# Performance work log

Measured on AMD Instinct MI355X. Metric: run time of the kernel, lower is better.

Reference implementation:

```python
import jax, jax.numpy as jnp
import numpy as np

BORDER_POWER = 0.5
BORDER_WEIGHT = 1.0


def _distance_transform(targets):
    """Vertical two-pass (grassfire) min-plus distance transform along H.

    Matches torch: init penalty=H everywhere, 0 at target==1, then a downward
    pass d[i] = min(d[i], d[i-1]+1) followed by an upward pass
    d[i] = min(d[i], d[i+1]+1).
    """
    H = targets.shape[2]
    D = jnp.where(targets == 1, jnp.float32(0.0), jnp.float32(H))  # (N,C,H,W)
    Dh = jnp.moveaxis(D, 2, 0)  # (H, N, C, W)

    def step(carry, row):
        r = jnp.minimum(row, carry + 1.0)
        return r, r

    big = jnp.full_like(Dh[0], jnp.inf)  # inf+1=inf so first row is unchanged
    _, Dfwd = jax.lax.scan(step, big, Dh)
    _, Dbwd = jax.lax.scan(step, big, Dfwd, reverse=True)
    return jnp.moveaxis(Dbwd, 0, 2)  # back to (N,C,H,W)


def setup_inputs() -> dict:
    key = jax.random.key(0)
    k1, k2 = jax.random.split(key)
    predictions = jax.random.normal(k1, (32, 1, 1024, 1024), dtype=jnp.float32)
    targets = jax.random.randint(k2, (32, 1, 1024, 1024), 0, 2).astype(jnp.float32)
    return {"predictions": predictions, "targets": targets}


def reference(predictions, targets):
    # BCEWithLogitsLoss, mean reduction (numerically stable form)
    bce = jnp.mean(
        jnp.maximum(predictions, 0.0)
        - predictions * targets
        + jnp.log1p(jnp.exp(-jnp.abs(predictions)))
    )

    # Border criterion: hard-thresholded sigmoid predictions times distance map
    pred_bin = (jax.nn.sigmoid(predictions) > 0.5).astype(jnp.float32)
    dist = _distance_transform(targets)
    penalty = pred_bin * dist
    total = penalty.sum()
    count = jnp.sum(penalty != 0).astype(jnp.float32)
    border = jnp.where(total == 0, 0.0, total / jnp.maximum(count, 1.0))

    return bce + BORDER_WEIGHT * border ** BORDER_POWER
```

## Files before the change

### kernel.cpp

```cpp
#include <hip/hip_runtime.h>
#include <math.h>

#define HH   1024
#define WW   1024
#define NIMG 32
#define NBLK (NIMG * (WW / 32))
#define NT   512
#define BIGD (1<<20)
#define L2E  1.44269504088896340736f

#if __has_builtin(__builtin_amdgcn_exp2f)
#define EXP2F(x) __builtin_amdgcn_exp2f(x)
#else
#define EXP2F(x) exp2f(x)
#endif
#if __has_builtin(__builtin_amdgcn_logf)
#define LOG2F(x) __builtin_amdgcn_logf(x)
#else
#define LOG2F(x) log2f(x)
#endif


__global__ __launch_bounds__(NT, 8) void dtl_main(const float* __restrict__ pred,
                                                  const float* __restrict__ tgt,
                                                  double* __restrict__ bceP,
                                                  unsigned* __restrict__ totP,
                                                  unsigned* __restrict__ cntP) {
    __shared__ unsigned long long nibw[16][64];
    __shared__ int st_first[16][32];
    __shared__ int st_last[16][32];
    __shared__ float    red_f[NT];
    __shared__ unsigned red_t[NT];
    __shared__ unsigned red_c[NT];

    const int tid   = threadIdx.x;
    const int lane  = tid & 63;
    const int wv    = tid >> 6;
    const int n     = blockIdx.x >> 5;
    const int strip = blockIdx.x & 31;

    const int rlow = lane & 7;
    const int quad = lane >> 3;
    const size_t f4base = ((size_t)n * HH + (size_t)(wv * 128 + rlow)) * (WW / 4)
                        + (size_t)(strip * 8 + quad);
    const float4* Pp = (const float4*)pred + f4base;
    const float4* Tp = (const float4*)tgt  + f4base;

    float bsum = 0.f;
    unsigned long long nv = 0ull;

    float4 pa = Pp[0],    ta = Tp[0];
    float4 pb = Pp[2048], tb = Tp[2048];

#pragma unroll 2
    for (int k = 0; k < 16; ++k) {
        const unsigned kn = (k < 14) ? (unsigned)((k + 2) * 2048) : 0u;
        const float4 pc = Pp[kn];
        const float4 tc = Tp[kn];

        const float c0 = fmaf(ta.x, -2.f * L2E, L2E);
        const float c1 = fmaf(ta.y, -2.f * L2E, L2E);
        const float c2 = fmaf(ta.z, -2.f * L2E, L2E);
        const float c3 = fmaf(ta.w, -2.f * L2E, L2E);
        const float z0 = EXP2F(c0 * pa.x);
        const float z1 = EXP2F(c1 * pa.y);
        const float z2 = EXP2F(c2 * pa.z);
        const float z3 = EXP2F(c3 * pa.w);
        const float w0  = 1.f + z0;
        const float w01 = fmaf(w0, z1, w0);
        const float w2  = 1.f + z2;
        const float w23 = fmaf(w2, z3, w2);
        bsum += LOG2F(w01 * w23);

        const unsigned tn = (unsigned)ta.x | ((unsigned)ta.y << 1) |
                            ((unsigned)ta.z << 2) | ((unsigned)ta.w << 3);
        const unsigned pn = (pa.x > 0.f ? 1u : 0u) | (pa.y > 0.f ? 2u : 0u) |
                            (pa.z > 0.f ? 4u : 0u) | (pa.w > 0.f ? 8u : 0u);
        nv |= (unsigned long long)(tn | (pn << 4)) << (8 * (k & 7));
        if ((k & 7) == 7) {
            nibw[wv * 2 + (k >> 3)][quad * 8 + rlow] = nv;
            nv = 0ull;
        }
        pa = pb; ta = tb; pb = pc; tb = tc;
    }
    __syncthreads();

    const int c   = tid & 31;
    const int q   = tid >> 5;
    const int h0  = q * 64;
    const int qs  = (c >> 2) * 8;
    const int tsh = c & 3;

    unsigned long long tw = 0ull, pw = 0ull;
#pragma unroll
    for (int r = 0; r < 8; ++r) {
        const unsigned long long x  = nibw[q][qs + r];
        const unsigned long long tb2 = (x >> tsh)       & 0x0101010101010101ULL;
        const unsigned long long pb2 = (x >> (4 + tsh)) & 0x0101010101010101ULL;
        tw |= tb2 << r;
        pw |= pb2 << r;
    }

    const int first = tw ? __builtin_ctzll(tw) : -1;
    const int last  = tw ? (63 - __builtin_clzll(tw)) : -1;
    st_first[q][c] = first;
    st_last[q][c]  = last;
    __syncthreads();

    int U = BIGD;
    for (int k = q - 1; k >= 0; --k) {
        const int l2 = st_last[k][c];
        if (l2 >= 0) { U = (h0 - 1) - (k * 64 + l2); break; }
    }
    int nxt_below = BIGD;
    for (int k = q + 1; k < 16; ++k) {
        const int fs = st_first[k][c];
        if (fs >= 0) { nxt_below = k * 64 + fs; break; }
    }

    int f   = U;
    int nxt = (first >= 0) ? (h0 + first) : nxt_below;
    unsigned tot = 0u, cnt = 0u;

#pragma unroll 4
    for (int b = 0; b < 64; ++b) {
        const int h = h0 + b;
        const int t = (int)((tw >> b) & 1ull);
        f = t ? 0 : (f + 1);
        if (h > nxt) {
            const unsigned long long m = tw & (~0ull << b);
            nxt = m ? (h0 + __builtin_ctzll(m)) : nxt_below;
        }
        int d = nxt - h;
        d = (f < d) ? f : d;
        d = (d < HH) ? d : HH;
        if (((pw >> b) & 1ull) && d > 0) { tot += (unsigned)d; cnt += 1u; }
    }

    red_f[tid] = bsum; red_t[tid] = tot; red_c[tid] = cnt;
    __syncthreads();
    for (int off = NT / 2; off > 0; off >>= 1) {
        if (tid < off) {
            red_f[tid] += red_f[tid + off];
            red_t[tid] += red_t[tid + off];
            red_c[tid] += red_c[tid + off];
        }
        __syncthreads();
    }
    if (tid == 0) {
        bceP[blockIdx.x] = (double)red_f[0];
        totP[blockIdx.x] = red_t[0];
        cntP[blockIdx.x] = red_c[0];
    }
}

__global__ __launch_bounds__(512) void dtl_final(const double* __restrict__ bceP,
                                                 const unsigned* __restrict__ totP,
                                                 const unsigned* __restrict__ cntP,
                                                 float* __restrict__ out) {
    __shared__ double             rf[512];
    __shared__ unsigned long long rt[512];
    __shared__ unsigned           rc[512];
    const int t = threadIdx.x;
    rf[t] = bceP[t] + bceP[t + 512];
    rt[t] = (unsigned long long)totP[t] + (unsigned long long)totP[t + 512];
    rc[t] = cntP[t] + cntP[t + 512];
    __syncthreads();
    for (int off = 256; off > 0; off >>= 1) {
        if (t < off) { rf[t] += rf[t + off]; rt[t] += rt[t + off]; rc[t] += rc[t + off]; }
        __syncthreads();
    }
    if (t == 0) {
        const double LN2 = 0.69314718055994530942;
        const double bce = LN2 * rf[0] / (double)((size_t)NIMG * HH * WW);
        double border = 0.0;
        if (rt[0] != 0ull) {
            const unsigned cc = (rc[0] > 1u) ? rc[0] : 1u;
            border = sqrt((double)rt[0] / (double)cc);
        }
        out[0] = (float)(bce + border);
    }
}

extern "C" void kernel_launch(void* const* d_in, const int* in_sizes, int n_in,
                              void* d_out, int out_size, void* d_ws, size_t ws_size,
                              hipStream_t stream) {
    const float* pred = (const float*)d_in[0];
    const float* tgt  = (const float*)d_in[1];
    float* out = (float*)d_out;

    double*   bceP = (double*)d_ws;
    unsigned* totP = (unsigned*)((char*)d_ws + 8192);
    unsigned* cntP = totP + NBLK;

    dtl_main<<<NBLK, NT, 0, stream>>>(pred, tgt, bceP, totP, cntP);
    dtl_final<<<1, 512, 0, stream>>>(bceP, totP, cntP, out);
}
```

Measured before the change: 67.18 us.

## Replace per-row distance scan with bitwise dilation, shuffle reductions, paired log

The per-column distance loop over 64 rows becomes a bit-parallel dilation: each iteration grows the target mask by one row and popcounts the still-unreached predicted pixels, so the total distance comes out as a sum of popcounts. The LDS tree reduction becomes wavefront shuffles plus an 8-entry combine, and the load loop handles two rows per iteration so one log2 covers eight elements. The dilation loop's trip count depends on the data (the largest distance in the column), and merging more terms into one log2 product raises the risk of overflow or precision loss.

```diff
diff --git a/kernel.cpp b/kernel.cpp
--- a/kernel.cpp
+++ b/kernel.cpp
@@ -29,9 +29,8 @@
     __shared__ unsigned long long nibw[16][64];
     __shared__ int st_first[16][32];
     __shared__ int st_last[16][32];
-    __shared__ float    red_f[NT];
-    __shared__ unsigned red_t[NT];
-    __shared__ unsigned red_c[NT];
+    __shared__ float    rfw[8];
+    __shared__ unsigned rtw[8], rcw[8];
 
     const int tid   = threadIdx.x;
     const int lane  = tid & 63;
@@ -52,36 +51,48 @@
     float4 pa = Pp[0],    ta = Tp[0];
     float4 pb = Pp[2048], tb = Tp[2048];
 
-#pragma unroll 2
-    for (int k = 0; k < 16; ++k) {
-        const unsigned kn = (k < 14) ? (unsigned)((k + 2) * 2048) : 0u;
-        const float4 pc = Pp[kn];
-        const float4 tc = Tp[kn];
-
-        const float c0 = fmaf(ta.x, -2.f * L2E, L2E);
-        const float c1 = fmaf(ta.y, -2.f * L2E, L2E);
-        const float c2 = fmaf(ta.z, -2.f * L2E, L2E);
-        const float c3 = fmaf(ta.w, -2.f * L2E, L2E);
-        const float z0 = EXP2F(c0 * pa.x);
-        const float z1 = EXP2F(c1 * pa.y);
-        const float z2 = EXP2F(c2 * pa.z);
-        const float z3 = EXP2F(c3 * pa.w);
-        const float w0  = 1.f + z0;
-        const float w01 = fmaf(w0, z1, w0);
-        const float w2  = 1.f + z2;
-        const float w23 = fmaf(w2, z3, w2);
-        bsum += LOG2F(w01 * w23);
-
-        const unsigned tn = (unsigned)ta.x | ((unsigned)ta.y << 1) |
-                            ((unsigned)ta.z << 2) | ((unsigned)ta.w << 3);
-        const unsigned pn = (pa.x > 0.f ? 1u : 0u) | (pa.y > 0.f ? 2u : 0u) |
-                            (pa.z > 0.f ? 4u : 0u) | (pa.w > 0.f ? 8u : 0u);
-        nv |= (unsigned long long)(tn | (pn << 4)) << (8 * (k & 7));
-        if ((k & 7) == 7) {
+#pragma unroll 1
+    for (int k = 0; k < 16; k += 2) {
+        const unsigned kn0 = (k < 14) ? (unsigned)((k + 2) * 2048) : 0u;
+        const unsigned kn1 = (k < 14) ? (unsigned)((k + 3) * 2048) : 0u;
+        const float4 pc = Pp[kn0], tc = Tp[kn0];
+        const float4 pd = Pp[kn1], td = Tp[kn1];
+
+        const float a0 = EXP2F(fmaf(ta.x, -2.f * L2E, L2E) * pa.x);
+        const float a1 = EXP2F(fmaf(ta.y, -2.f * L2E, L2E) * pa.y);
+        const float a2 = EXP2F(fmaf(ta.z, -2.f * L2E, L2E) * pa.z);
+        const float a3 = EXP2F(fmaf(ta.w, -2.f * L2E, L2E) * pa.w);
+        const float wa0 = 1.f + a0;
+        const float wa01 = fmaf(wa0, a1, wa0);
+        const float wa2 = 1.f + a2;
+        const float wa23 = fmaf(wa2, a3, wa2);
+
+        const float b0 = EXP2F(fmaf(tb.x, -2.f * L2E, L2E) * pb.x);
+        const float b1 = EXP2F(fmaf(tb.y, -2.f * L2E, L2E) * pb.y);
+        const float b2 = EXP2F(fmaf(tb.z, -2.f * L2E, L2E) * pb.z);
+        const float b3 = EXP2F(fmaf(tb.w, -2.f * L2E, L2E) * pb.w);
+        const float wb0 = 1.f + b0;
+        const float wb01 = fmaf(wb0, b1, wb0);
+        const float wb2 = 1.f + b2;
+        const float wb23 = fmaf(wb2, b3, wb2);
+
+        bsum += LOG2F((wa01 * wa23) * (wb01 * wb23));
+
+        const unsigned tna = (unsigned)ta.x | ((unsigned)ta.y << 1) |
+                             ((unsigned)ta.z << 2) | ((unsigned)ta.w << 3);
+        const unsigned pna = (pa.x > 0.f ? 1u : 0u) | (pa.y > 0.f ? 2u : 0u) |
+                             (pa.z > 0.f ? 4u : 0u) | (pa.w > 0.f ? 8u : 0u);
+        const unsigned tnb = (unsigned)tb.x | ((unsigned)tb.y << 1) |
+                             ((unsigned)tb.z << 2) | ((unsigned)tb.w << 3);
+        const unsigned pnb = (pb.x > 0.f ? 1u : 0u) | (pb.y > 0.f ? 2u : 0u) |
+                             (pb.z > 0.f ? 4u : 0u) | (pb.w > 0.f ? 8u : 0u);
+        nv |= (unsigned long long)(tna | (pna << 4)) << (8 * (k & 7));
+        nv |= (unsigned long long)(tnb | (pnb << 4)) << (8 * ((k + 1) & 7));
+        if (((k + 1) & 7) == 7) {
             nibw[wv * 2 + (k >> 3)][quad * 8 + rlow] = nv;
             nv = 0ull;
         }
-        pa = pb; ta = tb; pb = pc; tb = tc;
+        pa = pc; ta = tc; pb = pd; tb = td;
     }
     __syncthreads();
 
@@ -94,7 +105,7 @@
     unsigned long long tw = 0ull, pw = 0ull;
 #pragma unroll
     for (int r = 0; r < 8; ++r) {
-        const unsigned long long x  = nibw[q][qs + r];
+        const unsigned long long x   = nibw[q][qs + r];
         const unsigned long long tb2 = (x >> tsh)       & 0x0101010101010101ULL;
         const unsigned long long pb2 = (x >> (4 + tsh)) & 0x0101010101010101ULL;
         tw |= tb2 << r;
@@ -118,39 +129,39 @@
         if (fs >= 0) { nxt_below = k * 64 + fs; break; }
     }
 
-    int f   = U;
-    int nxt = (first >= 0) ? (h0 + first) : nxt_below;
-    unsigned tot = 0u, cnt = 0u;
-
-#pragma unroll 4
-    for (int b = 0; b < 64; ++b) {
-        const int h = h0 + b;
-        const int t = (int)((tw >> b) & 1ull);
-        f = t ? 0 : (f + 1);
-        if (h > nxt) {
-            const unsigned long long m = tw & (~0ull << b);
-            nxt = m ? (h0 + __builtin_ctzll(m)) : nxt_below;
+    const unsigned cnt = (unsigned)__popcll(pw & ~tw);
+
+    unsigned tot = 0u;
+    {
+        unsigned long long T = tw, ma = 0ull, mb = 0ull;
+        const int nbm64 = nxt_below - h0 - 64;
+        unsigned long long m = pw & ~T;
+        for (int k = 0; (k < HH) && m; ++k) {
+            tot += (unsigned)__popcll(m);
+            T |= (T << 1) | (T >> 1);
+            ma = (ma << 1) | ((k >= U) ? 1ull : 0ull);
+            mb = (mb >> 1) | ((k >= nbm64) ? 0x8000000000000000ull : 0ull);
+            m &= ~(T | ma | mb);
         }
-        int d = nxt - h;
-        d = (f < d) ? f : d;
-        d = (d < HH) ? d : HH;
-        if (((pw >> b) & 1ull) && d > 0) { tot += (unsigned)d; cnt += 1u; }
-    }
-
-    red_f[tid] = bsum; red_t[tid] = tot; red_c[tid] = cnt;
-    __syncthreads();
-    for (int off = NT / 2; off > 0; off >>= 1) {
-        if (tid < off) {
-            red_f[tid] += red_f[tid + off];
-            red_t[tid] += red_t[tid + off];
-            red_c[tid] += red_c[tid + off];
-        }
-        __syncthreads();
-    }
+    }
+
+    float rv = bsum;
+    unsigned vt = tot, vc = cnt;
+#pragma unroll
+    for (int o = 32; o > 0; o >>= 1) {
+        rv += __shfl_down(rv, o);
+        vt += __shfl_down(vt, o);
+        vc += __shfl_down(vc, o);
+    }
+    if (lane == 0) { rfw[wv] = rv; rtw[wv] = vt; rcw[wv] = vc; }
+    __syncthreads();
     if (tid == 0) {
-        bceP[blockIdx.x] = (double)red_f[0];
-        totP[blockIdx.x] = red_t[0];
-        cntP[blockIdx.x] = red_c[0];
+        float sf = 0.f; unsigned st = 0u, sc = 0u;
+#pragma unroll
+        for (int i = 0; i < 8; ++i) { sf += rfw[i]; st += rtw[i]; sc += rcw[i]; }
+        bceP[blockIdx.x] = (double)sf;
+        totP[blockIdx.x] = st;
+        cntP[blockIdx.x] = sc;
     }
 }
 
```

After: 55.27 us, median of 2. 1.22x faster.
